# Kernel optimization log

Hardware: AMD Instinct MI355X
Metric: run time of the kernel (lower is better)

The kernel has to match this reference:

```python
import jax, jax.numpy as jnp
import numpy as np

B, L, D, H = 4, 2048, 1024, 16
HD = D // H  # head dim = 64


def setup_inputs() -> dict:
    key = jax.random.key(0)
    ks = jax.random.split(key, 8)
    std_qkv = np.sqrt(D + D // H).astype(np.float32)  # matches nn.init.normal_ std in source
    xav = np.sqrt(2.0 / (D + D)).astype(np.float32)   # xavier_normal_ for fc_out
    return {
        "query": jax.random.normal(ks[0], (B, L, D), dtype=jnp.float32),
        "key": jax.random.normal(ks[1], (B, L, D), dtype=jnp.float32),
        "value": jax.random.normal(ks[2], (B, L, D), dtype=jnp.float32),
        "Wq": jax.random.normal(ks[3], (D, D), dtype=jnp.float32) * std_qkv,
        "Wk": jax.random.normal(ks[4], (D, D), dtype=jnp.float32) * std_qkv,
        "Wv": jax.random.normal(ks[5], (D, D), dtype=jnp.float32) * std_qkv,
        "Wo": jax.random.normal(ks[6], (D, D), dtype=jnp.float32) * xav,
        "bo": jnp.zeros((D,), dtype=jnp.float32),
    }


def reference(query, key, value, Wq, Wk, Wv, Wo, bo):
    # Linear projections (torch Linear: x @ W.T), then split heads: b l (h k) -> b h l k
    def split_heads(x):
        b, l, _ = x.shape
        return x.reshape(b, l, H, HD).transpose(0, 2, 1, 3)

    q = split_heads(query @ Wq.T)   # [B,H,L,HD]
    k = split_heads(key @ Wk.T)     # [B,H,T,HD]
    v = split_heads(value @ Wv.T)   # [B,H,T,HD]

    scale = 1.0 / np.sqrt(HD).astype(np.float32)
    energy = jnp.einsum("bhlk,bhtk->bhlt", q, k) * scale  # [B,H,L,T]
    attention = jax.nn.softmax(energy, axis=3)
    out = jnp.einsum("bhlt,bhtv->bhlv", attention, v)     # [B,H,L,HD]
    # b h l v -> b l (h v)
    out = out.transpose(0, 2, 1, 3).reshape(B, L, D)
    out = out @ Wo.T + bo  # dropout_rate=0.0 -> identity
    return out, attention
```

## Files before the change

kernel.cpp:

```cpp
#include <hip/hip_runtime.h>
#include <math.h>

#define Bb 4
#define Ls 2048
#define Dd 1024
#define Hh 16
#define HDm 64
#define ML (Bb*Ls)

typedef double f64x4 __attribute__((ext_vector_type(4)));
typedef float  f32x4 __attribute__((ext_vector_type(4)));
typedef short  bf16x8 __attribute__((ext_vector_type(8)));
typedef unsigned int u32;
typedef unsigned short u16;

__device__ __forceinline__ void gload16(const void* g, void* l) {
  __builtin_amdgcn_global_load_lds(
      (const __attribute__((address_space(1))) u32*)g,
      (__attribute__((address_space(3))) u32*)l, 16, 0, 0);
}

__device__ __forceinline__ u16 f2bf(float f) {
  u32 u = __float_as_uint(f);
  u += 0x7FFFu + ((u >> 16) & 1u);
  return (u16)(u >> 16);
}

__device__ __forceinline__ void gemm_core_nt(
    const float* __restrict__ A, const float* __restrict__ B,
    int bm, int bn, int w, int lrow, int lk, f64x4 acc[4]) {
  const int K = Dd;
  __shared__ __align__(16) float As[2][64 * 16];
  __shared__ __align__(16) float Bs[2][64 * 16];
  const int tid = threadIdx.x;
  const int r = tid >> 2, blk = tid & 3;
  const int sblk = blk ^ ((r >> 1) & 3);
  const int sxw = ((lrow >> 1) & 3) << 2;
  const float* ga = A + (size_t)(bm + r) * K + 4 * sblk;
  const float* gb = B + (size_t)(bn + r) * K + 4 * sblk;

#pragma unroll
  for (int j = 0; j < 4; j++) acc[j] = (f64x4){0., 0., 0., 0.};

  char* la0 = (char*)&As[0][0] + w * 1024;
  char* lb0 = (char*)&Bs[0][0] + w * 1024;
  char* la1 = (char*)&As[1][0] + w * 1024;
  char* lb1 = (char*)&Bs[1][0] + w * 1024;

  gload16(ga, la0);
  gload16(gb, lb0);
  __syncthreads();

  int cur = 0;
  for (int k0 = 16; k0 <= K; k0 += 16) {
    if (k0 < K) {
      gload16(ga + k0, cur ? la0 : la1);
      gload16(gb + k0, cur ? lb0 : lb1);
    }
    const float* Abuf = &As[cur][0];
    const float* Bbuf = &Bs[cur][0];
#pragma unroll
    for (int t = 0; t < 4; t++) {
      double a = (double)Abuf[(16 * w + lrow) * 16 + ((4 * t + lk) ^ sxw)];
#pragma unroll
      for (int j = 0; j < 4; j++) {
        double bv = (double)Bbuf[(16 * j + lrow) * 16 + ((4 * t + lk) ^ sxw)];
        acc[j] = __builtin_amdgcn_mfma_f64_16x16x4f64(a, bv, acc[j], 0, 0, 0);
      }
    }
    __syncthreads();
    cur ^= 1;
  }
}

__global__ __launch_bounds__(256) void gemm_nt_mfma_f64(
    const float* __restrict__ A, const float* __restrict__ B,
    double* __restrict__ C, double outscale) {
  const int tid = threadIdx.x;
  const int lane = tid & 63;
  const int w = tid >> 6;
  const int lrow = lane & 15, lk = lane >> 4;
  const int bm = blockIdx.y * 64, bn = blockIdx.x * 64;
  f64x4 acc[4];
  gemm_core_nt(A, B, bm, bn, w, lrow, lk, acc);
#pragma unroll
  for (int j = 0; j < 4; j++)
#pragma unroll
    for (int d = 0; d < 4; d++) {
      size_t m = (size_t)(bm + 16 * w + 4 * d + lk);
      C[m * Dd + bn + 16 * j + lrow] = acc[j][d] * outscale;
    }
}

__global__ __launch_bounds__(256) void gemm_nt_mfma_f32(
    const float* __restrict__ A, const float* __restrict__ B,
    const float* __restrict__ bias, float* __restrict__ C) {
  const int tid = threadIdx.x;
  const int lane = tid & 63;
  const int w = tid >> 6;
  const int lrow = lane & 15, lk = lane >> 4;
  const int bm = blockIdx.y * 64, bn = blockIdx.x * 64;
  f64x4 acc[4];
  gemm_core_nt(A, B, bm, bn, w, lrow, lk, acc);
#pragma unroll
  for (int j = 0; j < 4; j++)
#pragma unroll
    for (int d = 0; d < 4; d++) {
      size_t m = (size_t)(bm + 16 * w + 4 * d + lk);
      int n = bn + 16 * j + lrow;
      float v = (float)acc[j][d];
      if (bias) v += bias[n];
      C[m * Dd + n] = v;
    }
}

__global__ __launch_bounds__(256) void gemm_nt_mfma_bf16o(
    const float* __restrict__ A, const float* __restrict__ B,
    u16* __restrict__ C) {
  const int tid = threadIdx.x;
  const int lane = tid & 63;
  const int w = tid >> 6;
  const int lrow = lane & 15, lk = lane >> 4;
  const int bm = blockIdx.y * 64, bn = blockIdx.x * 64;
  f64x4 acc[4];
  gemm_core_nt(A, B, bm, bn, w, lrow, lk, acc);
#pragma unroll
  for (int j = 0; j < 4; j++)
#pragma unroll
    for (int d = 0; d < 4; d++) {
      size_t m = (size_t)(bm + 16 * w + 4 * d + lk);
      C[m * Dd + bn + 16 * j + lrow] = f2bf((float)acc[j][d]);
    }
}

__global__ __launch_bounds__(256) void attn_flash(
    double* __restrict__ Qd, const double* __restrict__ Kd,
    const u16* __restrict__ Vf, float* __restrict__ attn,
    float* __restrict__ O) {
  __shared__ __align__(16) double Kbuf[2][32 * 64];
  __shared__ __align__(16) u16    Vb16[2][32 * 64];
  __shared__ __align__(16) u16    Pb[4][16 * 32];
  __shared__ __align__(16) float  Fs[4][16];

  const int tid = threadIdx.x;
  const int lane = tid & 63;
  const int w = tid >> 6;
  const int lrow = lane & 15;
  const int lk = lane >> 4;
  const int blk = blockIdx.x;
  const int qt = blk & 31;
  const int h = (blk >> 5) & 15;
  const int b = blk >> 9;
  const int l0 = qt * 64;

  const double* Qg = Qd + ((size_t)(b * Ls + l0)) * Dd + h * HDm;
  const double* Kg = Kd + ((size_t)b * Ls) * Dd + h * HDm;
  const u16*    Vg = Vf + ((size_t)b * Ls) * Dd + h * HDm;
  float* aout = attn + ((size_t)((b * Hh + h) * Ls + l0)) * Ls;

  double qreg[16];
#pragma unroll
  for (int t = 0; t < 16; t++)
    qreg[t] = Qg[(size_t)(16 * w + lrow) * Dd + 4 * t + lk];

  const int l16 = (lane & 31) * 16;
  const int halfk = lane >> 5;
  const int sx = (lrow & 7) << 1;

  auto stage = [&](int kts, int bsel) {
#pragma unroll
    for (int jj = 0; jj < 4; jj++) {
      int i = w + 4 * jj;
      int row = 2 * i + halfk;
      int inner = l16 ^ ((row & 7) << 4);
      const char* g = (const char*)Kg + (((size_t)(kts * 32 + row)) << 13) + inner;
      gload16(g, (char*)(&Kbuf[bsel][0]) + i * 1024);
    }
    {
      const char* g = (const char*)Vg +
          ((size_t)(kts * 32 + 8 * w + (lane >> 3))) * (Dd * 2) + (lane & 7) * 16;
      gload16(g, (char*)(&Vb16[bsel][0]) + w * 1024);
    }
  };

  float mreff[4];
  double sacc[4];
  f32x4 pacc[4];
#pragma unroll
  for (int d = 0; d < 4; d++) {
    mreff[d] = -INFINITY;
    sacc[d] = 0.0;
    pacc[d] = (f32x4){0.f, 0.f, 0.f, 0.f};
  }

  stage(0, 0);
  __syncthreads();

  int cur = 0;
  for (int kt = 0; kt < 64; kt++) {
    if (kt < 63) stage(kt + 1, cur ^ 1);

    const double* Kb = &Kbuf[cur][0];

    f64x4 acc0 = {0.0, 0.0, 0.0, 0.0};
    f64x4 acc1 = {0.0, 0.0, 0.0, 0.0};
#pragma unroll
    for (int t = 0; t < 16; t++) {
      int ko = (4 * t + lk) ^ sx;
      double b0 = Kb[lrow * 64 + ko];
      double b1 = Kb[(16 + lrow) * 64 + ko];
      acc0 = __builtin_amdgcn_mfma_f64_16x16x4f64(qreg[t], b0, acc0, 0, 0, 0);
      acc1 = __builtin_amdgcn_mfma_f64_16x16x4f64(qreg[t], b1, acc1, 0, 0, 0);
    }

#pragma unroll
    for (int d = 0; d < 4; d++) {
      double e0 = acc0[d];
      double e1 = acc1[d];
      float tmf = fmaxf((float)e0, (float)e1);
#pragma unroll
      for (int m = 1; m < 16; m <<= 1) tmf = fmaxf(tmf, __shfl_xor(tmf, m));
      float mo_f = mreff[d];
      float ref_f = fmaxf(mo_f, tmf);
      double ref = (double)ref_f;
      float p0 = expf((float)(e0 - ref));
      float p1 = expf((float)(e1 - ref));
      double ts = (double)p0 + (double)p1;
#pragma unroll
      for (int m = 1; m < 16; m <<= 1) ts += __shfl_xor(ts, m);
      float factor = expf(mo_f - ref_f);
      sacc[d] = sacc[d] * (double)factor + ts;
      mreff[d] = ref_f;
      int row = 16 * w + 4 * d + lk;
      aout[(size_t)row * Ls + kt * 32 + lrow] = p0;
      aout[(size_t)row * Ls + kt * 32 + 16 + lrow] = p1;
      if (lrow == 0) {
        ((float*)(Qd + ((size_t)(b * Ls + l0 + row)) * Dd + h * HDm))[kt] = ref_f;
        Fs[w][4 * d + lk] = factor;
      }
      Pb[w][(4 * d + lk) * 32 + lrow] = f2bf(p0);
      Pb[w][(4 * d + lk) * 32 + 16 + lrow] = f2bf(p1);
    }

    bf16x8 afr = *(const bf16x8*)&Pb[w][lrow * 32 + 8 * lk];
    f32x4 fv = *(const f32x4*)&Fs[w][4 * lk];
    const u16* Vb = &Vb16[cur][0];
#pragma unroll
    for (int q = 0; q < 4; q++) {
      pacc[q][0] *= fv[0];
      pacc[q][1] *= fv[1];
      pacc[q][2] *= fv[2];
      pacc[q][3] *= fv[3];
      bf16x8 bfr;
#pragma unroll
      for (int r = 0; r < 8; r++)
        bfr[r] = (short)Vb[(8 * lk + r) * 64 + 16 * q + lrow];
      pacc[q] = __builtin_amdgcn_mfma_f32_16x16x32_bf16(afr, bfr, pacc[q], 0, 0, 0);
    }

    __syncthreads();
    cur ^= 1;
  }

  if (lrow == 0) {
#pragma unroll
    for (int d = 0; d < 4; d++) Fs[w][4 * d + lk] = (float)(1.0 / sacc[d]);
  }
  f32x4 sv = *(const f32x4*)&Fs[w][4 * lk];
#pragma unroll
  for (int q = 0; q < 4; q++)
#pragma unroll
    for (int r = 0; r < 4; r++) {
      int row = 16 * w + 4 * lk + r;
      O[((size_t)(b * Ls + l0 + row)) * Dd + h * HDm + 16 * q + lrow] =
          pacc[q][r] * sv[r];
    }
  if (lrow == 0) {
#pragma unroll
    for (int d = 0; d < 4; d++) {
      int row = 16 * w + 4 * d + lk;
      float* mrow = (float*)(Qd + ((size_t)(b * Ls + l0 + row)) * Dd + h * HDm);
      mrow[64] = mreff[d];
      *(double*)(mrow + 66) = sacc[d];
    }
  }
}

__global__ __launch_bounds__(256) void attn_scale(
    float* __restrict__ attn, const double* __restrict__ Qd) {
  int R = blockIdx.x;
  int b = R >> 15;
  int rem = R & 32767;
  int h = rem >> 11;
  int l = rem & 2047;
  const float* mrow = (const float*)(Qd + ((size_t)(b * Ls + l)) * Dd + h * HDm);
  int tid = threadIdx.x;
  int kt = tid >> 2;
  double mt = (double)mrow[kt];
  double mf = (double)mrow[64];
  double s = *(const double*)(mrow + 66);
  float sc = (float)(exp(mt - mf) / s);
  float4* ap = (float4*)(attn + (size_t)R * Ls + tid * 8);
  float4 a0 = ap[0], a1 = ap[1];
  a0.x *= sc; a0.y *= sc; a0.z *= sc; a0.w *= sc;
  a1.x *= sc; a1.y *= sc; a1.z *= sc; a1.w *= sc;
  ap[0] = a0; ap[1] = a1;
}

extern "C" void kernel_launch(void* const* d_in, const int* in_sizes, int n_in,
                              void* d_out, int out_size, void* d_ws, size_t ws_size,
                              hipStream_t stream) {
  const float* query = (const float*)d_in[0];
  const float* key   = (const float*)d_in[1];
  const float* value = (const float*)d_in[2];
  const float* Wq    = (const float*)d_in[3];
  const float* Wk    = (const float*)d_in[4];
  const float* Wv    = (const float*)d_in[5];
  const float* Wo    = (const float*)d_in[6];
  const float* bo    = (const float*)d_in[7];

  float* out0 = (float*)d_out;
  float* attn = out0 + (size_t)ML * Dd;

  char* ws = (char*)d_ws;
  double* Qd  = (double*)ws;
  double* Kd  = (double*)(ws + (size_t)ML * Dd * 8);
  u16*    Vfb = (u16*)(ws + (size_t)ML * Dd * 16);
  float*  Of  = (float*)(ws + (size_t)ML * Dd * 16 + (size_t)ML * Dd * 2);

  dim3 gemm_grid(Dd / 64, ML / 64);
  gemm_nt_mfma_f64<<<gemm_grid, 256, 0, stream>>>(query, Wq, Qd, 0.125);
  gemm_nt_mfma_f64<<<gemm_grid, 256, 0, stream>>>(key,   Wk, Kd, 1.0);
  gemm_nt_mfma_bf16o<<<gemm_grid, 256, 0, stream>>>(value, Wv, Vfb);

  attn_flash<<<Bb * Hh * (Ls / 64), 256, 0, stream>>>(Qd, Kd, Vfb, attn, Of);
  attn_scale<<<Bb * Hh * Ls, 256, 0, stream>>>(attn, Qd);

  gemm_nt_mfma_f32<<<gemm_grid, 256, 0, stream>>>(Of, Wo, bo, out0);
}
```

Baseline: 3.969 ms.

## Run V and output projections as bf16 MFMA GEMMs instead of f64

Converts value, Wv and Wo to bf16 in separate conversion kernels and replaces the f64-MFMA GEMMs for the V projection and the output projection with a new bf16 MFMA GEMM that accumulates in f32. The attention kernel now writes its output in bf16 so the final projection can read it directly. This is meant to remove the cost of slow f64 matrix instructions and to halve GEMM input bandwidth. In exchange it adds three conversion passes and lowers the precision of V and of the final output.

Measured after the change: 3.459 ms. 12.8% less time.

```diff
diff --git a/kernel.cpp b/kernel.cpp
--- a/kernel.cpp
+++ b/kernel.cpp
@@ -24,6 +24,18 @@
   u32 u = __float_as_uint(f);
   u += 0x7FFFu + ((u >> 16) & 1u);
   return (u16)(u >> 16);
+}
+
+__global__ __launch_bounds__(256) void f32_to_bf16(
+    const float* __restrict__ in, u16* __restrict__ out, int n8) {
+  int i = blockIdx.x * 256 + threadIdx.x;
+  if (i >= n8) return;
+  const float4* p = (const float4*)(in + (size_t)i * 8);
+  float4 a = p[0], c = p[1];
+  union { u16 h[8]; uint4 v; } o;
+  o.h[0] = f2bf(a.x); o.h[1] = f2bf(a.y); o.h[2] = f2bf(a.z); o.h[3] = f2bf(a.w);
+  o.h[4] = f2bf(c.x); o.h[5] = f2bf(c.y); o.h[6] = f2bf(c.z); o.h[7] = f2bf(c.w);
+  *(uint4*)(out + (size_t)i * 8) = o.v;
 }
 
 __device__ __forceinline__ void gemm_core_nt(
@@ -92,51 +104,69 @@
     }
 }
 
-__global__ __launch_bounds__(256) void gemm_nt_mfma_f32(
-    const float* __restrict__ A, const float* __restrict__ B,
-    const float* __restrict__ bias, float* __restrict__ C) {
+__global__ __launch_bounds__(256) void gemm_nt_bf16(
+    const u16* __restrict__ A, const u16* __restrict__ B,
+    const float* __restrict__ bias, u16* __restrict__ Cb,
+    float* __restrict__ Cf) {
+  const int K = Dd;
+  __shared__ __align__(16) u16 Asb[2][64 * 32];
+  __shared__ __align__(16) u16 Bsb[2][64 * 32];
   const int tid = threadIdx.x;
   const int lane = tid & 63;
   const int w = tid >> 6;
   const int lrow = lane & 15, lk = lane >> 4;
   const int bm = blockIdx.y * 64, bn = blockIdx.x * 64;
-  f64x4 acc[4];
-  gemm_core_nt(A, B, bm, bn, w, lrow, lk, acc);
+
+  const int srow = 16 * w + (lane >> 2);
+  const u16* ga = A + (size_t)(bm + srow) * K + 8 * (lane & 3);
+  const u16* gb = B + (size_t)(bn + srow) * K + 8 * (lane & 3);
+  char* la0 = (char*)&Asb[0][0] + w * 1024;
+  char* lb0 = (char*)&Bsb[0][0] + w * 1024;
+  char* la1 = (char*)&Asb[1][0] + w * 1024;
+  char* lb1 = (char*)&Bsb[1][0] + w * 1024;
+
+  f32x4 acc[4] = {{0.f,0.f,0.f,0.f},{0.f,0.f,0.f,0.f},
+                  {0.f,0.f,0.f,0.f},{0.f,0.f,0.f,0.f}};
+
+  gload16(ga, la0);
+  gload16(gb, lb0);
+  __syncthreads();
+
+  int cur = 0;
+  for (int k0 = 32; k0 <= K; k0 += 32) {
+    if (k0 < K) {
+      gload16(ga + k0, cur ? la0 : la1);
+      gload16(gb + k0, cur ? lb0 : lb1);
+    }
+    const u16* Ab = &Asb[cur][0];
+    const u16* Bt = &Bsb[cur][0];
+    bf16x8 afr = *(const bf16x8*)&Ab[(16 * w + lrow) * 32 + 8 * lk];
+#pragma unroll
+    for (int j = 0; j < 4; j++) {
+      bf16x8 bfr = *(const bf16x8*)&Bt[(16 * j + lrow) * 32 + 8 * lk];
+      acc[j] = __builtin_amdgcn_mfma_f32_16x16x32_bf16(afr, bfr, acc[j], 0, 0, 0);
+    }
+    __syncthreads();
+    cur ^= 1;
+  }
+
 #pragma unroll
   for (int j = 0; j < 4; j++)
 #pragma unroll
-    for (int d = 0; d < 4; d++) {
-      size_t m = (size_t)(bm + 16 * w + 4 * d + lk);
+    for (int r = 0; r < 4; r++) {
+      size_t m = (size_t)(bm + 16 * w + 4 * lk + r);
       int n = bn + 16 * j + lrow;
-      float v = (float)acc[j][d];
+      float v = acc[j][r];
       if (bias) v += bias[n];
-      C[m * Dd + n] = v;
-    }
-}
-
-__global__ __launch_bounds__(256) void gemm_nt_mfma_bf16o(
-    const float* __restrict__ A, const float* __restrict__ B,
-    u16* __restrict__ C) {
-  const int tid = threadIdx.x;
-  const int lane = tid & 63;
-  const int w = tid >> 6;
-  const int lrow = lane & 15, lk = lane >> 4;
-  const int bm = blockIdx.y * 64, bn = blockIdx.x * 64;
-  f64x4 acc[4];
-  gemm_core_nt(A, B, bm, bn, w, lrow, lk, acc);
-#pragma unroll
-  for (int j = 0; j < 4; j++)
-#pragma unroll
-    for (int d = 0; d < 4; d++) {
-      size_t m = (size_t)(bm + 16 * w + 4 * d + lk);
-      C[m * Dd + bn + 16 * j + lrow] = f2bf((float)acc[j][d]);
+      if (Cf) Cf[m * Dd + n] = v;
+      else    Cb[m * Dd + n] = f2bf(v);
     }
 }
 
 __global__ __launch_bounds__(256) void attn_flash(
     double* __restrict__ Qd, const double* __restrict__ Kd,
     const u16* __restrict__ Vf, float* __restrict__ attn,
-    float* __restrict__ O) {
+    u16* __restrict__ O) {
   __shared__ __align__(16) double Kbuf[2][32 * 64];
   __shared__ __align__(16) u16    Vb16[2][32 * 64];
   __shared__ __align__(16) u16    Pb[4][16 * 32];
@@ -273,7 +303,7 @@
     for (int r = 0; r < 4; r++) {
       int row = 16 * w + 4 * lk + r;
       O[((size_t)(b * Ls + l0 + row)) * Dd + h * HDm + 16 * q + lrow] =
-          pacc[q][r] * sv[r];
+          f2bf(pacc[q][r] * sv[r]);
     }
   if (lrow == 0) {
 #pragma unroll
@@ -323,18 +353,28 @@
   float* attn = out0 + (size_t)ML * Dd;
 
   char* ws = (char*)d_ws;
-  double* Qd  = (double*)ws;
-  double* Kd  = (double*)(ws + (size_t)ML * Dd * 8);
-  u16*    Vfb = (u16*)(ws + (size_t)ML * Dd * 16);
-  float*  Of  = (float*)(ws + (size_t)ML * Dd * 16 + (size_t)ML * Dd * 2);
+  double* Qd   = (double*)ws;
+  double* Kd   = (double*)(ws + (size_t)ML * Dd * 8);
+  u16*    Vfb  = (u16*)(ws + (size_t)ML * Dd * 16);
+  u16*    Ofb  = (u16*)(ws + (size_t)ML * Dd * 16 + (size_t)ML * Dd * 2);
+  u16*    valb = (u16*)(ws + (size_t)ML * Dd * 16 + (size_t)ML * Dd * 4);
+  u16*    Wvb  = (u16*)(ws + (size_t)ML * Dd * 16 + (size_t)ML * Dd * 6);
+  u16*    Wob  = (u16*)(ws + (size_t)ML * Dd * 16 + (size_t)ML * Dd * 6
+                           + (size_t)Dd * Dd * 2);
 
   dim3 gemm_grid(Dd / 64, ML / 64);
+
+  f32_to_bf16<<<(ML * Dd / 8) / 256, 256, 0, stream>>>(value, valb, ML * Dd / 8);
+  f32_to_bf16<<<(Dd * Dd / 8) / 256, 256, 0, stream>>>(Wv, Wvb, Dd * Dd / 8);
+  f32_to_bf16<<<(Dd * Dd / 8) / 256, 256, 0, stream>>>(Wo, Wob, Dd * Dd / 8);
+
   gemm_nt_mfma_f64<<<gemm_grid, 256, 0, stream>>>(query, Wq, Qd, 0.125);
   gemm_nt_mfma_f64<<<gemm_grid, 256, 0, stream>>>(key,   Wk, Kd, 1.0);
-  gemm_nt_mfma_bf16o<<<gemm_grid, 256, 0, stream>>>(value, Wv, Vfb);
-
-  attn_flash<<<Bb * Hh * (Ls / 64), 256, 0, stream>>>(Qd, Kd, Vfb, attn, Of);
+
+  gemm_nt_bf16<<<gemm_grid, 256, 0, stream>>>(valb, Wvb, nullptr, Vfb, nullptr);
+
+  attn_flash<<<Bb * Hh * (Ls / 64), 256, 0, stream>>>(Qd, Kd, Vfb, attn, Ofb);
   attn_scale<<<Bb * Hh * Ls, 256, 0, stream>>>(attn, Qd);
 
-  gemm_nt_mfma_f32<<<gemm_grid, 256, 0, stream>>>(Of, Wo, bo, out0);
-}
+  gemm_nt_bf16<<<gemm_grid, 256, 0, stream>>>(Ofb, Wob, bo, nullptr, out0);
+}
```
